# Performance work log

Measured on AMD Instinct MI355X. Metric: run time of the kernel, lower is better.

Reference implementation:

```python
import jax, jax.numpy as jnp
import numpy as np

KERNEL_LEN = 512
INPUT_LEN = 65536


def setup_inputs() -> dict:
    key = jax.random.key(0)
    k1, k2 = jax.random.split(key)
    x = jax.random.normal(k1, (INPUT_LEN,), dtype=jnp.float32)
    kernel = jax.random.normal(k2, (KERNEL_LEN,), dtype=jnp.float32)
    return {"input": x, "kernel": kernel}


def _dtw_row(prev, d_row):
    # prev: accumulated_cost of previous row, shape [K]
    # ac[j] = min(prev[j-1], prev[j], ac[j-1]) + d[j]
    # Let c[j] = min(prev[j-1], prev[j]) + d[j]  (prev[-1] treated as +inf,
    # which reproduces ac[i,0] = prev[0] + d[0]).
    # Then ac[j] = min(c[j], ac[j-1] + d[j])
    #            = S[j] + cummin_k<=j (c[k] - S[k]),  S = inclusive cumsum of d.
    inf = jnp.full((1,), jnp.inf, dtype=d_row.dtype)
    prev_shift = jnp.concatenate([inf, prev[:-1]])
    c = jnp.minimum(prev_shift, prev) + d_row
    S = jnp.cumsum(d_row)
    ac = S + jax.lax.cummin(c - S)
    return ac, ac[-1]


def reference(input, kernel):
    # pairwise squared distances: [input_len, kernel_len]
    d = (kernel[None, :] - input[:, None]) ** 2
    # row 0: cumulative sum along kernel axis
    prev0 = jnp.cumsum(d[0])
    # rows 1..N-1 via scan with wavefront-free min-plus row update
    _, lasts = jax.lax.scan(_dtw_row, prev0, d[1:])
    # return accumulated_cost[:, kernel_len - 1]
    return jnp.concatenate([prev0[-1:], lasts])
```

## Files before the change

### kernel.cpp

```cpp
#include <hip/hip_runtime.h>


#define K_LEN 512
#define N_LEN 65536
#define PAD_L 512
#define PAD_R 1024
#define XPAD_TOTAL (PAD_L + N_LEN + PAD_R)
#define BIGX 1e20f
#define NCHUNK 1032
#define RING 256

typedef float f32x2 __attribute__((ext_vector_type(2)));

__global__ void dtw_pad_kernel(const float* __restrict__ x, float* __restrict__ xpad) {
    int i = blockIdx.x * blockDim.x + threadIdx.x;
    if (i < XPAD_TOTAL) {
        int j = i - PAD_L;
        xpad[i] = (j >= 0 && j < N_LEN) ? x[j] : BIGX;
    }
}

__device__ __forceinline__ float dpp_wave_shr1(float oldv, float src) {
    return __int_as_float(__builtin_amdgcn_update_dpp(
        __float_as_int(oldv), __float_as_int(src), 0x138, 0xF, 0xF, false));
}
__device__ __forceinline__ float dpp_wave_shl1(float oldv, float src) {
    return __int_as_float(__builtin_amdgcn_update_dpp(
        __float_as_int(oldv), __float_as_int(src), 0x130, 0xF, 0xF, false));
}

#define BARRIER() asm volatile("s_waitcnt lgkmcnt(0)\n\ts_barrier" ::: "memory")
#define WAITV16() do { asm volatile("s_waitcnt vmcnt(16)" ::: "memory"); \
                       __builtin_amdgcn_sched_barrier(0); } while (0)

struct XB { f32x2 v[8]; };

__device__ __forceinline__ void load_sb(XB& b, const float* p) {
    asm volatile(
        "global_load_dwordx2 %0, %[ad], off\n\t"
        "global_load_dwordx2 %1, %[ad], off offset:8\n\t"
        "global_load_dwordx2 %2, %[ad], off offset:16\n\t"
        "global_load_dwordx2 %3, %[ad], off offset:24\n\t"
        "global_load_dwordx2 %4, %[ad], off offset:32\n\t"
        "global_load_dwordx2 %5, %[ad], off offset:40\n\t"
        "global_load_dwordx2 %6, %[ad], off offset:48\n\t"
        "global_load_dwordx2 %7, %[ad], off offset:56"
        : "=v"(b.v[0]), "=v"(b.v[1]), "=v"(b.v[2]), "=v"(b.v[3]),
          "=v"(b.v[4]), "=v"(b.v[5]), "=v"(b.v[6]), "=v"(b.v[7])
        : [ad] "v"(p)
        : "memory");
}

template <bool LAST>
__device__ __forceinline__ void run_loop(const float* __restrict__ xl,
                                         const float* __restrict__ ldsIn,
                                         float* __restrict__ ldsOut,
                                         float* __restrict__ lds,
                                         float k0, float k1, int lane, int tid,
                                         float* __restrict__ out) {
    const float INFV = __builtin_inff();
    float A0 = INFV, A0p = INFV, A1 = INFV, E1 = INFV;
    float xp = xl[-1];

    XB b0, b1, b2, b3;
    float bk;

    auto ITER = [&](float xf) {
        const float esh0 = dpp_wave_shr1(bk, E1);
        const float t0v = k0 - xf;
        const float na0 = __builtin_fmaf(t0v, t0v, fminf(A0, esh0));
        const float t1v = k1 - xp;
        const float m1  = fminf(A0p, fminf(A1, A0));
        const float na1 = __builtin_fmaf(t1v, t1v, m1);
        const float ne1 = fminf(na1, A1);
        bk = dpp_wave_shl1(LAST ? na1 : ne1, bk);
        A0p = A0; A0 = na0; A1 = na1; E1 = ne1; xp = xf;
    };
    auto COMPUTE = [&](const XB& b) {
#pragma unroll
        for (int q = 0; q < 8; ++q) { ITER(b.v[q].x); ITER(b.v[q].y); }
    };

    load_sb(b0, xl);
    load_sb(b1, xl + 16);


    for (int c = 0; c < NCHUNK; ++c) {
        const int t0 = c * 64;
        const int rb = (c & 3) << 6;
        bk = ldsIn[(rb + lane - 1) & (RING - 1)];

        load_sb(b2, xl + t0 + 32); WAITV16(); COMPUTE(b0);
        load_sb(b3, xl + t0 + 48); WAITV16(); COMPUTE(b1);
        load_sb(b0, xl + t0 + 64); WAITV16(); COMPUTE(b2);
        load_sb(b1, xl + t0 + 80); WAITV16(); COMPUTE(b3);

        if (!LAST) {
            ldsOut[rb + lane] = bk;
        } else {
            const int oi = t0 + lane - (K_LEN - 1);
            if (oi >= 0 && oi < N_LEN) out[oi] = bk;
        }
        if (c == 0 && tid == 0) lds[4 * RING - 1] = INFV;
        BARRIER();
    }
}

__global__ __launch_bounds__(256, 1) void dtw_main(const float* __restrict__ xpad,
                                                   const float* __restrict__ kern,
                                                   float* __restrict__ out) {
    __shared__ float lds[4 * RING];
    const float INFV = __builtin_inff();
    const int tid  = threadIdx.x;
    const int w    = __builtin_amdgcn_readfirstlane(tid) >> 6;
    const int lane = tid & 63;

    for (int i = tid; i < 4 * RING; i += 256)
        lds[i] = (i == 4 * RING - 1) ? 0.0f : INFV;
    __syncthreads();

    const int j0 = w * 128 + 2 * lane;
    const float k0 = kern[j0];
    const float k1 = kern[j0 + 1];

    const float* xl = xpad + (PAD_L - j0);

    float* ldsOut      = lds + w * RING;
    const float* ldsIn = (w == 0) ? (lds + 3 * RING) : (lds + (w - 1) * RING);

    for (int b = 0; b < w; ++b) BARRIER();

    if (w == 3)
        run_loop<true >(xl, ldsIn, ldsOut, lds, k0, k1, lane, tid, out);
    else
        run_loop<false>(xl, ldsIn, ldsOut, lds, k0, k1, lane, tid, out);

    for (int b = 0; b < 3 - w; ++b) BARRIER();
}

extern "C" void kernel_launch(void* const* d_in, const int* in_sizes, int n_in,
                              void* d_out, int out_size, void* d_ws, size_t ws_size,
                              hipStream_t stream) {
    const float* x = (const float*)d_in[0];
    const float* k = (const float*)d_in[1];
    float* xpad = (float*)d_ws;
    float* out  = (float*)d_out;
    dtw_pad_kernel<<<(XPAD_TOTAL + 255) / 256, 256, 0, stream>>>(x, xpad);
    dtw_main<<<1, 256, 0, stream>>>(xpad, k, out);
}
```

Baseline: 2.328 ms.

## Use eight waves with one kernel column per lane and DPP-streamed inputs

Splits the 512 kernel columns over eight waves with one column per lane, where before four waves each handled two columns per lane. Each lane now does a single global load per 64-row chunk. Within the chunk, input samples are passed across lanes with DPP row shifts, replacing the inline-asm multi-buffered global loads. The goal is to place two waves on each SIMD so the serial min-plus dependency chain can interleave and hide latency. In exchange it adds two extra DPP operations per row, a longer inter-wave pipeline with more barrier stages, and a wider ring buffer in LDS.

```diff
diff --git a/kernel.cpp b/kernel.cpp
--- a/kernel.cpp
+++ b/kernel.cpp
@@ -9,8 +9,7 @@
 #define BIGX 1e20f
 #define NCHUNK 1032
 #define RING 256
-
-typedef float f32x2 __attribute__((ext_vector_type(2)));
+#define NW 8
 
 __global__ void dtw_pad_kernel(const float* __restrict__ x, float* __restrict__ xpad) {
     int i = blockIdx.x * blockDim.x + threadIdx.x;
@@ -30,112 +29,82 @@
 }
 
 #define BARRIER() asm volatile("s_waitcnt lgkmcnt(0)\n\ts_barrier" ::: "memory")
-#define WAITV16() do { asm volatile("s_waitcnt vmcnt(16)" ::: "memory"); \
-                       __builtin_amdgcn_sched_barrier(0); } while (0)
 
-struct XB { f32x2 v[8]; };
-
-__device__ __forceinline__ void load_sb(XB& b, const float* p) {
-    asm volatile(
-        "global_load_dwordx2 %0, %[ad], off\n\t"
-        "global_load_dwordx2 %1, %[ad], off offset:8\n\t"
-        "global_load_dwordx2 %2, %[ad], off offset:16\n\t"
-        "global_load_dwordx2 %3, %[ad], off offset:24\n\t"
-        "global_load_dwordx2 %4, %[ad], off offset:32\n\t"
-        "global_load_dwordx2 %5, %[ad], off offset:40\n\t"
-        "global_load_dwordx2 %6, %[ad], off offset:48\n\t"
-        "global_load_dwordx2 %7, %[ad], off offset:56"
-        : "=v"(b.v[0]), "=v"(b.v[1]), "=v"(b.v[2]), "=v"(b.v[3]),
-          "=v"(b.v[4]), "=v"(b.v[5]), "=v"(b.v[6]), "=v"(b.v[7])
-        : [ad] "v"(p)
-        : "memory");
+template <bool LAST>
+__device__ __forceinline__ float chunk64(float bk, float xf, float& xc,
+                                         float& A, float& E, float k) {
+#pragma unroll
+    for (int r = 0; r < 64; ++r) {
+        xc = dpp_wave_shr1(xf, xc);
+        xf = dpp_wave_shl1(xf, xf);
+        const float esh = dpp_wave_shr1(bk, E);
+        const float tv  = k - xc;
+        const float nA  = __builtin_fmaf(tv, tv, fminf(A, esh));
+        const float nE  = fminf(nA, A);
+        bk = dpp_wave_shl1(LAST ? nA : nE, bk);
+        A = nA; E = nE;
+    }
+    return bk;
 }
 
 template <bool LAST>
-__device__ __forceinline__ void run_loop(const float* __restrict__ xl,
-                                         const float* __restrict__ ldsIn,
-                                         float* __restrict__ ldsOut,
-                                         float* __restrict__ lds,
-                                         float k0, float k1, int lane, int tid,
-                                         float* __restrict__ out) {
+__device__ __forceinline__ void run_all(const float* __restrict__ xb,
+                                        const float* __restrict__ ldsIn,
+                                        float* __restrict__ ldsOut,
+                                        float* __restrict__ lds,
+                                        float k, int lane, int tid,
+                                        float* __restrict__ out) {
     const float INFV = __builtin_inff();
-    float A0 = INFV, A0p = INFV, A1 = INFV, E1 = INFV;
-    float xp = xl[-1];
-
-    XB b0, b1, b2, b3;
-    float bk;
-
-    auto ITER = [&](float xf) {
-        const float esh0 = dpp_wave_shr1(bk, E1);
-        const float t0v = k0 - xf;
-        const float na0 = __builtin_fmaf(t0v, t0v, fminf(A0, esh0));
-        const float t1v = k1 - xp;
-        const float m1  = fminf(A0p, fminf(A1, A0));
-        const float na1 = __builtin_fmaf(t1v, t1v, m1);
-        const float ne1 = fminf(na1, A1);
-        bk = dpp_wave_shl1(LAST ? na1 : ne1, bk);
-        A0p = A0; A0 = na0; A1 = na1; E1 = ne1; xp = xf;
-    };
-    auto COMPUTE = [&](const XB& b) {
-#pragma unroll
-        for (int q = 0; q < 8; ++q) { ITER(b.v[q].x); ITER(b.v[q].y); }
-    };
-
-    load_sb(b0, xl);
-    load_sb(b1, xl + 16);
-
+    float xc = BIGX;
+    float A = INFV, E = INFV;
+    float fcur = xb[0];
 
     for (int c = 0; c < NCHUNK; ++c) {
-        const int t0 = c * 64;
         const int rb = (c & 3) << 6;
-        bk = ldsIn[(rb + lane - 1) & (RING - 1)];
-
-        load_sb(b2, xl + t0 + 32); WAITV16(); COMPUTE(b0);
-        load_sb(b3, xl + t0 + 48); WAITV16(); COMPUTE(b1);
-        load_sb(b0, xl + t0 + 64); WAITV16(); COMPUTE(b2);
-        load_sb(b1, xl + t0 + 80); WAITV16(); COMPUTE(b3);
-
+        const float fnext = xb[(c + 1) * 64];
+        float bk = ldsIn[(rb + lane - 1) & (RING - 1)];
+        bk = chunk64<LAST>(bk, fcur, xc, A, E, k);
         if (!LAST) {
             ldsOut[rb + lane] = bk;
         } else {
-            const int oi = t0 + lane - (K_LEN - 1);
+            const int oi = c * 64 + lane - (K_LEN - 1);
             if (oi >= 0 && oi < N_LEN) out[oi] = bk;
         }
-        if (c == 0 && tid == 0) lds[4 * RING - 1] = INFV;
+        if (c == 0 && tid == 0) lds[7 * RING + RING - 1] = INFV;
         BARRIER();
+        fcur = fnext;
     }
 }
 
-__global__ __launch_bounds__(256, 1) void dtw_main(const float* __restrict__ xpad,
+__global__ __launch_bounds__(512, 1) void dtw_main(const float* __restrict__ xpad,
                                                    const float* __restrict__ kern,
                                                    float* __restrict__ out) {
-    __shared__ float lds[4 * RING];
+    __shared__ float lds[NW * RING];
     const float INFV = __builtin_inff();
     const int tid  = threadIdx.x;
     const int w    = __builtin_amdgcn_readfirstlane(tid) >> 6;
     const int lane = tid & 63;
 
-    for (int i = tid; i < 4 * RING; i += 256)
-        lds[i] = (i == 4 * RING - 1) ? 0.0f : INFV;
+    for (int i = tid; i < NW * RING; i += 512)
+        lds[i] = (i == 7 * RING + RING - 1) ? 0.0f : INFV;
     __syncthreads();
 
-    const int j0 = w * 128 + 2 * lane;
-    const float k0 = kern[j0];
-    const float k1 = kern[j0 + 1];
-
-    const float* xl = xpad + (PAD_L - j0);
+    const float k = kern[w * 64 + lane];
+    const float* xb = xpad + (PAD_L - w * 64) + lane;
 
     float* ldsOut      = lds + w * RING;
-    const float* ldsIn = (w == 0) ? (lds + 3 * RING) : (lds + (w - 1) * RING);
+    const float* ldsIn = (w == 0) ? (lds + 7 * RING) : (lds + (w - 1) * RING);
 
     for (int b = 0; b < w; ++b) BARRIER();
 
-    if (w == 3)
-        run_loop<true >(xl, ldsIn, ldsOut, lds, k0, k1, lane, tid, out);
+    if (w == 7)
+        run_all<true >(xb, ldsIn, ldsOut, lds, k, lane, tid, out);
     else
-        run_loop<false>(xl, ldsIn, ldsOut, lds, k0, k1, lane, tid, out);
+        run_all<false>(xb, ldsIn, ldsOut, lds, k, lane, tid, out);
 
-    for (int b = 0; b < 3 - w; ++b) BARRIER();
+    for (int b = 0; b < 7 - w; ++b) BARRIER();
+
+    (void)INFV;
 }
 
 extern "C" void kernel_launch(void* const* d_in, const int* in_sizes, int n_in,
@@ -146,5 +115,5 @@
     float* xpad = (float*)d_ws;
     float* out  = (float*)d_out;
     dtw_pad_kernel<<<(XPAD_TOTAL + 255) / 256, 256, 0, stream>>>(x, xpad);
-    dtw_main<<<1, 256, 0, stream>>>(xpad, k, out);
+    dtw_main<<<1, 512, 0, stream>>>(xpad, k, out);
 }
```

After: 2.711 ms. 16.4% more time.
